# Optimization experiments

Measured on AMD Instinct MI355X. Metric: run time of the kernel, lower is better.

## Reference

```python
import jax, jax.numpy as jnp
import numpy as np

# graph structure constants
G = 64            # num graphs
NPG = 1600        # nodes per graph
N = G * NPG       # 102400 total nodes
EPG = 51200       # edges per graph (avg degree 32)
E = G * EPG       # 3276800 total edges
F_IN = 512
H_OUT = 512
RATIO = 0.8
K = int(np.ceil(RATIO * NPG))   # 1280 kept nodes per graph
NK = G * K


def gcn_conv(x, src, dst, W, b, n, ew):
    """PyG GCNConv: D^-1/2 (A+I) D^-1/2 X W + b, with edge weights ew."""
    h = x @ W
    deg = jax.ops.segment_sum(ew, dst, num_segments=n) + 1.0  # +1 for self loop
    dis = jax.lax.rsqrt(deg)
    norm = dis[src] * dis[dst] * ew                 # [E]
    agg = jax.ops.segment_sum(h[src] * norm[:, None], dst, num_segments=n)
    return agg + h * (dis * dis)[:, None] + b       # self-loop norm = dis_i^2


def setup_inputs() -> dict:
    key = jax.random.key(0)
    k_x, k_e, k_w1, k_wr, k_wo, k_w2 = jax.random.split(key, 6)
    x = jax.random.normal(k_x, (N, F_IN), dtype=jnp.float32)
    # within-graph random edges
    local = jax.random.randint(k_e, (2, G, EPG), 0, NPG, dtype=jnp.int32)
    offs = (jnp.arange(G, dtype=jnp.int32) * NPG)[None, :, None]
    edge_index = (local + offs).reshape(2, E)
    batch = jnp.repeat(jnp.arange(G, dtype=jnp.int32), NPG)
    W1 = jax.random.normal(k_w1, (F_IN, 16), dtype=jnp.float32) * (1.0 / np.sqrt(F_IN))
    b1 = jnp.zeros((16,), jnp.float32)
    Wrel = jax.random.normal(k_wr, (16, 1), dtype=jnp.float32) * 0.25
    brel = jnp.zeros((1,), jnp.float32)
    Wroot = jax.random.normal(k_wo, (16, 1), dtype=jnp.float32) * 0.25
    W2 = jax.random.normal(k_w2, (16, H_OUT), dtype=jnp.float32) * 0.25
    b2 = jnp.zeros((H_OUT,), jnp.float32)
    return {"x": x, "edge_index": edge_index, "batch": batch,
            "W1": W1, "b1": b1, "Wrel": Wrel, "brel": brel,
            "Wroot": Wroot, "W2": W2, "b2": b2}


def reference(x, edge_index, batch, W1, b1, Wrel, brel, Wroot, W2, b2):
    src, dst = edge_index[0], edge_index[1]
    ones_e = jnp.ones((E,), x.dtype)
    # conv1 + relu
    h1 = jax.nn.relu(gcn_conv(x, src, dst, W1, b1, N, ones_e))   # [N,16]
    # SAGPooling score: GraphConv(16,1) = lin_rel(sum_j x_j) + lin_root(x), then tanh
    agg = jax.ops.segment_sum(h1[src], dst, num_segments=N)
    score = jnp.tanh((agg @ Wrel + brel + h1 @ Wroot)[:, 0])      # [N]
    # per-graph top-k (graphs are equal-sized, contiguous)
    vals, idx = jax.lax.top_k(score.reshape(G, NPG), K)           # [G,K]
    perm = (idx + (jnp.arange(G, dtype=idx.dtype) * NPG)[:, None]).reshape(-1)  # [NK]
    xk = h1[perm] * vals.reshape(-1)[:, None]                     # x[perm] * score[perm]
    # filter_adj: keep edges with both endpoints kept, remap indices
    kept = jnp.zeros((N,), bool).at[perm].set(True)
    inv = jnp.zeros((N,), jnp.int32).at[perm].set(jnp.arange(NK, dtype=jnp.int32))
    em = (kept[src] & kept[dst]).astype(x.dtype)                  # weight-0 == dropped edge
    # conv2 + relu on pooled graph
    h2 = jax.nn.relu(gcn_conv(xk, inv[src], inv[dst], W2, b2, NK, em))  # [NK,H]
    # global mean pool (each graph keeps exactly K nodes)
    out = jax.ops.segment_sum(h2, batch[perm], num_segments=G) / K
    return out
```

## Files before the change

kernel.cpp:

```cpp
#include <hip/hip_runtime.h>
#include <math.h>

#define G_    64
#define NPG_  1600
#define N_    (G_*NPG_)
#define EPG_  51200
#define E_    (G_*EPG_)
#define FIN_  512
#define HOUT_ 512
#define KEEP_ 1280

__global__ __launch_bounds__(1024) void k_build(const int* __restrict__ esrc,
                                                const int* __restrict__ edst,
                                                int* __restrict__ offs,
                                                int* __restrict__ rend,
                                                float* __restrict__ dis,
                                                unsigned short* __restrict__ csr) {
  __shared__ __align__(16) unsigned short csrs[EPG_];
  __shared__ int hist[NPG_];
  __shared__ int wsum[16];
  const int g = blockIdx.x, t = threadIdx.x;
  const int lane = t & 63, wid = t >> 6;
  const int eb = g * EPG_, nb = g * NPG_;

  for (int i = t; i < NPG_; i += 1024) hist[i] = 0;
  __syncthreads();
  for (int e = t; e < EPG_; e += 1024) atomicAdd(&hist[edst[eb + e] - nb], 1);
  __syncthreads();

  int c0 = 0, c1 = 0;
  if (t < 800) { c0 = hist[2 * t]; c1 = hist[2 * t + 1]; }
  const int val = c0 + c1;
  int incl = val;
#pragma unroll
  for (int m = 1; m < 64; m <<= 1) {
    const int u = __shfl_up(incl, m);
    if (lane >= m) incl += u;
  }
  if (lane == 63) wsum[wid] = incl;
  __syncthreads();
  int woff = 0;
  for (int w2 = 0; w2 < wid; ++w2) woff += wsum[w2];
  incl += woff;
  if (t < 800) {
    const int excl = incl - val;
    const int p0 = excl, p1 = p0 + c0;
    offs[nb + 2 * t] = eb + p0;     rend[nb + 2 * t] = eb + p1;
    offs[nb + 2 * t + 1] = eb + p1; rend[nb + 2 * t + 1] = eb + p1 + c1;
    dis[nb + 2 * t] = rsqrtf((float)c0 + 1.0f);
    dis[nb + 2 * t + 1] = rsqrtf((float)c1 + 1.0f);
    hist[2 * t] = p0;
    hist[2 * t + 1] = p1;
  }
  __syncthreads();
  for (int e = t; e < EPG_; e += 1024) {
    const int s = esrc[eb + e];
    const int d = edst[eb + e] - nb;
    const int p = atomicAdd(&hist[d], 1);
    csrs[p] = (unsigned short)(s - nb);
  }
  __syncthreads();
  const uint4* s4 = reinterpret_cast<const uint4*>(csrs);
  uint4* d4 = reinterpret_cast<uint4*>(csr + eb);
  for (int i = t; i < EPG_ / 8; i += 1024) d4[i] = s4[i];
}

typedef _Float16 f16x8 __attribute__((ext_vector_type(8)));
typedef float f32x4 __attribute__((ext_vector_type(4)));
#define WSTR_ 520

__global__ __launch_bounds__(256, 4) void k_xw1(const float* __restrict__ x,
                                                const float* __restrict__ W1,
                                                const float* __restrict__ dis,
                                                float* __restrict__ hd) {
  __shared__ _Float16 wls[2][16][WSTR_];
  const int t = threadIdx.x;

  for (int i = t; i < FIN_ * 16; i += 256) {
    const int k = i >> 4, n = i & 15;
    const float w = W1[i];
    const _Float16 w1 = (_Float16)w;
    const float r = w - (float)w1;
    wls[0][n][k] = w1;
    wls[1][n][k] = (_Float16)r;
  }
  __syncthreads();

  const int lane = t & 63, wid = t >> 6;
  const int g = lane >> 4, m = lane & 15;
  const int tile = blockIdx.x * 4 + wid;
  const int rb = tile * 16;

  const float* xrow = x + (size_t)(rb + m) * FIN_ + g * 8;
  const _Float16* wb1 = &wls[0][m][g * 8];
  const _Float16* wb2 = &wls[1][m][g * 8];

  f32x4 acc = {0.f, 0.f, 0.f, 0.f};
#pragma unroll
  for (int t4 = 0; t4 < 16; ++t4) {
    const float4 p0 = *reinterpret_cast<const float4*>(xrow + t4 * 32);
    const float4 p1 = *reinterpret_cast<const float4*>(xrow + t4 * 32 + 4);
    const float xv[8] = {p0.x, p0.y, p0.z, p0.w, p1.x, p1.y, p1.z, p1.w};
    f16x8 a1, a2;
#pragma unroll
    for (int j = 0; j < 8; ++j) {
      const _Float16 h = (_Float16)xv[j];
      a1[j] = h;
      a2[j] = (_Float16)(xv[j] - (float)h);
    }
    const f16x8 b1 = *reinterpret_cast<const f16x8*>(wb1 + t4 * 32);
    const f16x8 b2 = *reinterpret_cast<const f16x8*>(wb2 + t4 * 32);
    acc = __builtin_amdgcn_mfma_f32_16x16x32_f16(a1, b1, acc, 0, 0, 0);
    acc = __builtin_amdgcn_mfma_f32_16x16x32_f16(a1, b2, acc, 0, 0, 0);
    acc = __builtin_amdgcn_mfma_f32_16x16x32_f16(a2, b1, acc, 0, 0, 0);
  }

  const float4 d4 = reinterpret_cast<const float4*>(dis)[(rb >> 2) + g];
  const float dd[4] = {d4.x, d4.y, d4.z, d4.w};
#pragma unroll
  for (int rg = 0; rg < 4; ++rg)
    hd[(size_t)(rb + g * 4 + rg) * 16 + m] = acc[rg] * dd[rg];
}

__global__ __launch_bounds__(1024) void k_conv1l(
    const unsigned short* __restrict__ csr, const int* __restrict__ offs,
    const int* __restrict__ rend, const float* __restrict__ hd,
    const float* __restrict__ dis, const float* __restrict__ b1,
    const float* __restrict__ Wrel, const float* __restrict__ Wroot,
    float* __restrict__ h1, float* __restrict__ rarr, float* __restrict__ tarr) {
  __shared__ float hds[NPG_ * 16];
  const int g = blockIdx.x >> 2, q = blockIdx.x & 3;
  const int nb = g * NPG_;
  const int t = threadIdx.x;
  {
    const float4* src = reinterpret_cast<const float4*>(hd + (size_t)nb * 16);
    float4* dst = reinterpret_cast<float4*>(hds);
    for (int i = t; i < NPG_ * 4; i += 1024) dst[i] = src[i];
  }
  __syncthreads();
  const int c = t & 15;
  const float bb = b1[c], wr = Wrel[c], wo = Wroot[c];
  const int vend = q * 400 + 400;
  for (int vl = q * 400 + (t >> 4); vl < vend; vl += 64) {
    const int v = nb + vl;
    const int rs = offs[v], re = rend[v];
    float acc = 0.f;
    int k = rs;
    for (; k + 4 <= re; k += 4) {
      const int s0 = csr[k], s1 = csr[k + 1];
      const int s2 = csr[k + 2], s3 = csr[k + 3];
      acc += hds[s0 * 16 + c] + hds[s1 * 16 + c];
      acc += hds[s2 * 16 + c] + hds[s3 * 16 + c];
    }
    for (; k < re; ++k) acc += hds[csr[k] * 16 + c];
    const float dd = dis[v];
    float val = fmaf(acc + hds[vl * 16 + c], dd, bb);
    val = fmaxf(val, 0.f);
    h1[(size_t)v * 16 + c] = val;
    float r = val * wr;
    float tt = val * wo;
#pragma unroll
    for (int m = 1; m < 16; m <<= 1) {
      r += __shfl_xor(r, m);
      tt += __shfl_xor(tt, m);
    }
    if (c == 0) { rarr[v] = r; tarr[v] = tt; }
  }
}

__global__ __launch_bounds__(1024) void k_scoretopk(
    const unsigned short* __restrict__ csr, const int* __restrict__ offs,
    const int* __restrict__ rend, const float* __restrict__ rarr,
    const float* __restrict__ tarr, const float* __restrict__ brel,
    const float* __restrict__ h1, int* __restrict__ kept,
    float* __restrict__ dis2, float* __restrict__ h1w,
    float* __restrict__ out) {
  __shared__ float rar[NPG_];
  __shared__ float sar[NPG_];
  __shared__ int   ofs[NPG_];
  __shared__ int   ren[NPG_];
  __shared__ unsigned uu[NPG_];
  __shared__ int   kp[NPG_];
  __shared__ float wv[NPG_];
  __shared__ int   hist[256];
  __shared__ int   part[16];
  __shared__ int   scal[2];

  const int g = blockIdx.x, t = threadIdx.x;
  const int lane = t & 63, wid = t >> 6;
  const int nb = g * NPG_;

  for (int i = t; i < NPG_; i += 1024) {
    rar[i] = rarr[nb + i];
    sar[i] = tarr[nb + i];
    ofs[i] = offs[nb + i];
    ren[i] = rend[nb + i];
  }
  if (t == 0) { scal[0] = 0; scal[1] = KEEP_; }
  __syncthreads();

  const float br = brel[0];
  for (int v = t; v < NPG_; v += 1024) {
    const int rs = ofs[v], re = ren[v];
    float sum = 0.f;
    int k = rs;
    for (; k + 4 <= re; k += 4) {
      sum += rar[csr[k]] + rar[csr[k + 1]];
      sum += rar[csr[k + 2]] + rar[csr[k + 3]];
    }
    for (; k < re; ++k) sum += rar[csr[k]];
    const float s = tanhf(sum + br + sar[v]);
    sar[v] = s;
    const unsigned ub = __float_as_uint(s);
    uu[v] = (ub & 0x80000000u) ? ~ub : (ub | 0x80000000u);
  }
  __syncthreads();

  const unsigned maskTab[4] = {0u, 0xFF000000u, 0xFFFF0000u, 0xFFFFFF00u};
  const int shTab[4] = {24, 16, 8, 0};
  for (int pass = 0; pass < 4; ++pass) {
    const unsigned lo = (unsigned)scal[0];
    const int remc = scal[1];
    const unsigned msk = maskTab[pass];
    const int sh = shTab[pass];
    if (t < 256) hist[t] = 0;
    __syncthreads();
    for (int v = t; v < NPG_; v += 1024) {
      const unsigned u = uu[v];
      if (((u ^ lo) & msk) == 0) atomicAdd(&hist[(u >> sh) & 255], 1);
    }
    __syncthreads();
    int hv = 0;
    if (t < 256) hv = hist[t];
    int incl = hv;
#pragma unroll
    for (int m = 1; m < 64; m <<= 1) {
      const int u2 = __shfl_up(incl, m);
      if (lane >= m) incl += u2;
    }
    if (t < 256 && lane == 63) part[wid] = incl;
    __syncthreads();
    if (t < 256) {
      int woff = 0;
      for (int w2 = 0; w2 < wid; ++w2) woff += part[w2];
      const int tot = part[0] + part[1] + part[2] + part[3];
      const int sb = tot - (incl + woff) + hv;
      const int sb1 = sb - hv;
      if (sb >= remc && sb1 < remc) {
        scal[0] = (int)(lo | ((unsigned)t << sh));
        scal[1] = remc - sb1;
      }
    }
    __syncthreads();
  }
  const unsigned T = (unsigned)scal[0];
  const int remT = scal[1];

  const int i0 = 2 * t, i1 = 2 * t + 1;
  int f0 = 0, f1 = 0;
  if (i0 < NPG_) f0 = (uu[i0] == T);
  if (i1 < NPG_) f1 = (uu[i1] == T);
  int incl2 = f0 + f1;
#pragma unroll
  for (int m = 1; m < 64; m <<= 1) {
    const int u2 = __shfl_up(incl2, m);
    if (lane >= m) incl2 += u2;
  }
  if (lane == 63) part[wid] = incl2;
  __syncthreads();
  int woff2 = 0;
  for (int w2 = 0; w2 < wid; ++w2) woff2 += part[w2];
  const int excl = incl2 + woff2 - (f0 + f1);
  if (i0 < NPG_) kp[i0] = (uu[i0] > T) || (f0 && excl < remT);
  if (i1 < NPG_) kp[i1] = (uu[i1] > T) || (f1 && (excl + f0) < remT);
  __syncthreads();
  for (int v = t; v < NPG_; v += 1024) kept[nb + v] = kp[v];

  for (int v = t; v < NPG_; v += 1024) {
    float w = 0.f;
    if (kp[v]) {
      const int rs = ofs[v], re = ren[v];
      int c2 = 0, k = rs;
      for (; k + 4 <= re; k += 4) {
        c2 += kp[csr[k]] + kp[csr[k + 1]];
        c2 += kp[csr[k + 2]] + kp[csr[k + 3]];
      }
      for (; k < re; ++k) c2 += kp[csr[k]];
      const float d2 = rsqrtf((float)c2 + 1.0f);
      dis2[nb + v] = d2;
      w = sar[v] * d2;
    }
    wv[v] = w;
  }
  if (t < HOUT_) out[g * HOUT_ + t] = 0.f;
  __syncthreads();

  for (int i = t; i < NPG_ * 16; i += 1024)
    h1w[(size_t)nb * 16 + i] = h1[(size_t)nb * 16 + i] * wv[i >> 4];
}

__global__ __launch_bounds__(1024) void k_conv2l(
    const unsigned short* __restrict__ csr, const int* __restrict__ offs,
    const int* __restrict__ rend, const float* __restrict__ h1w,
    const int* __restrict__ kept, const float* __restrict__ dis2,
    float* __restrict__ y16) {
  __shared__ float hds[NPG_ * 16];
  const int g = blockIdx.x >> 2, q = blockIdx.x & 3;
  const int nb = g * NPG_;
  const int t = threadIdx.x;
  {
    const float4* src = reinterpret_cast<const float4*>(h1w + (size_t)nb * 16);
    float4* dst = reinterpret_cast<float4*>(hds);
    for (int i = t; i < NPG_ * 4; i += 1024) dst[i] = src[i];
  }
  __syncthreads();
  const int c = t & 15;
  const int vend = q * 400 + 400;
  for (int vl = q * 400 + (t >> 4); vl < vend; vl += 64) {
    const int v = nb + vl;
    if (!kept[v]) continue;
    const int rs = offs[v], re = rend[v];
    float acc = 0.f;
    int k = rs;
    for (; k + 4 <= re; k += 4) {
      const int s0 = csr[k], s1 = csr[k + 1];
      const int s2 = csr[k + 2], s3 = csr[k + 3];
      acc += hds[s0 * 16 + c] + hds[s1 * 16 + c];
      acc += hds[s2 * 16 + c] + hds[s3 * 16 + c];
    }
    for (; k < re; ++k) acc += hds[csr[k] * 16 + c];
    acc += hds[vl * 16 + c];
    y16[(size_t)v * 16 + c] = acc * dis2[v];
  }
}

__global__ __launch_bounds__(256, 1) void k_gemm2pool(const float* __restrict__ y16,
                                                      const int* __restrict__ kept,
                                                      const float* __restrict__ W2,
                                                      const float* __restrict__ b2,
                                                      float* __restrict__ out) {
  __shared__ float red[256];
  const int blk = blockIdx.x;
  const int g = blk >> 5;
  const int sub = blk & 31;
  const int jbase = (sub & 1) * 256;
  const int nstart = g * NPG_ + (sub >> 1) * 100;
  const int tid = threadIdx.x;
  const int wave = tid >> 6, lane = tid & 63;

  float w[16][4];
#pragma unroll
  for (int k = 0; k < 16; ++k)
#pragma unroll
    for (int c = 0; c < 4; ++c)
      w[k][c] = W2[k * HOUT_ + jbase + lane + c * 64];
  float b2r[4];
#pragma unroll
  for (int c = 0; c < 4; ++c) b2r[c] = b2[jbase + lane + c * 64];

  float acc[4] = {0.f, 0.f, 0.f, 0.f};
  for (int i = wave; i < 100; i += 4) {
    const int v = nstart + i;
    if (!kept[v]) continue;
    const float4* yp = reinterpret_cast<const float4*>(y16 + (size_t)v * 16);
    float4 q0 = yp[0], q1 = yp[1], q2 = yp[2], q3 = yp[3];
    const float yv[16] = {q0.x, q0.y, q0.z, q0.w, q1.x, q1.y, q1.z, q1.w,
                          q2.x, q2.y, q2.z, q2.w, q3.x, q3.y, q3.z, q3.w};
    float z[4] = {b2r[0], b2r[1], b2r[2], b2r[3]};
#pragma unroll
    for (int k = 0; k < 16; ++k)
#pragma unroll
      for (int c = 0; c < 4; ++c)
        z[c] = fmaf(yv[k], w[k][c], z[c]);
#pragma unroll
    for (int c = 0; c < 4; ++c) acc[c] += fmaxf(z[c], 0.f);
  }

  red[tid] = 0.f;
  __syncthreads();
#pragma unroll
  for (int c = 0; c < 4; ++c) atomicAdd(&red[lane + 64 * c], acc[c]);
  __syncthreads();
  atomicAdd(&out[g * HOUT_ + jbase + tid], red[tid] * (1.0f / (float)KEEP_));
}

extern "C" void kernel_launch(void* const* d_in, const int* in_sizes, int n_in,
                              void* d_out, int out_size, void* d_ws, size_t ws_size,
                              hipStream_t stream) {
  (void)in_sizes; (void)n_in; (void)out_size; (void)ws_size;
  const float* x     = (const float*)d_in[0];
  const int*   ei    = (const int*)  d_in[1];
  const float* W1    = (const float*)d_in[3];
  const float* b1    = (const float*)d_in[4];
  const float* Wrel  = (const float*)d_in[5];
  const float* brel  = (const float*)d_in[6];
  const float* Wroot = (const float*)d_in[7];
  const float* W2    = (const float*)d_in[8];
  const float* b2    = (const float*)d_in[9];
  const int* esrc = ei;
  const int* edst = ei + E_;

  char* ws = (char*)d_ws;
  float*          hd    = (float*)(ws);
  float*          h1    = (float*)(ws + 6553600);
  float*          h1w   = (float*)(ws + 13107200);
  float*          y16   = (float*)(ws + 19660800);
  unsigned short* csr   = (unsigned short*)(ws + 26214400);
  int*            offs  = (int*)(ws + 32768000);
  int*            rendp = (int*)(ws + 33177600);
  float*          dis   = (float*)(ws + 33587200);
  int*            kept  = (int*)(ws + 33996800);
  float*          rarr  = (float*)(ws + 34406400);
  float*          tarr  = (float*)(ws + 34816000);
  float*          dis2  = (float*)(ws + 35225600);
  float*          out   = (float*)d_out;

  hipLaunchKernelGGL(k_build,     dim3(G_),    dim3(1024), 0, stream,
                     esrc, edst, offs, rendp, dis, csr);
  hipLaunchKernelGGL(k_xw1,       dim3(1600),  dim3(256),  0, stream,
                     x, W1, dis, hd);
  hipLaunchKernelGGL(k_conv1l,    dim3(256),   dim3(1024), 0, stream,
                     csr, offs, rendp, hd, dis, b1, Wrel, Wroot, h1, rarr, tarr);
  hipLaunchKernelGGL(k_scoretopk, dim3(G_),    dim3(1024), 0, stream,
                     csr, offs, rendp, rarr, tarr, brel, h1, kept, dis2, h1w, out);
  hipLaunchKernelGGL(k_conv2l,    dim3(256),   dim3(1024), 0, stream,
                     csr, offs, rendp, h1w, kept, dis2, y16);
  hipLaunchKernelGGL(k_gemm2pool, dim3(2048),  dim3(256),  0, stream,
                     y16, kept, W2, b2, out);
}
```

Measured before the change: 214.1 us.

## Split score/top-k kernel into score, top-k and post kernels across more blocks

The fused per-graph score/top-k kernel ran only 64 blocks, leaving most CUs idle during the edge-gather phases. It is now split into three kernels: a 320-block score kernel, a 64-block radix top-k kernel that works on precomputed keys, and a 320-block post kernel that computes the pooled-graph degree and scales h1. Scores and keys go through global memory in reused workspace (the hd region), and the change adds two kernel launches.

Result: no change. 214.3 us (+0.1%).

```diff
diff --git a/kernel.cpp b/kernel.cpp
--- a/kernel.cpp
+++ b/kernel.cpp
@@ -168,52 +168,47 @@
   }
 }
 
-__global__ __launch_bounds__(1024) void k_scoretopk(
+__global__ __launch_bounds__(320) void k_score(
     const unsigned short* __restrict__ csr, const int* __restrict__ offs,
     const int* __restrict__ rend, const float* __restrict__ rarr,
     const float* __restrict__ tarr, const float* __restrict__ brel,
-    const float* __restrict__ h1, int* __restrict__ kept,
-    float* __restrict__ dis2, float* __restrict__ h1w,
+    float* __restrict__ scoreg, unsigned* __restrict__ uug) {
+  __shared__ float rar[NPG_];
+  const int g = blockIdx.x / 5, q = blockIdx.x % 5;
+  const int nb = g * NPG_;
+  const int t = threadIdx.x;
+  for (int i = t; i < NPG_; i += 320) rar[i] = rarr[nb + i];
+  __syncthreads();
+  const int vl = q * 320 + t;
+  const int v = nb + vl;
+  const int rs = offs[v], re = rend[v];
+  float sum = 0.f;
+  int k = rs;
+  for (; k + 4 <= re; k += 4) {
+    sum += rar[csr[k]] + rar[csr[k + 1]];
+    sum += rar[csr[k + 2]] + rar[csr[k + 3]];
+  }
+  for (; k < re; ++k) sum += rar[csr[k]];
+  const float s = tanhf(sum + brel[0] + tarr[v]);
+  scoreg[v] = s;
+  const unsigned ub = __float_as_uint(s);
+  uug[v] = (ub & 0x80000000u) ? ~ub : (ub | 0x80000000u);
+}
+
+__global__ __launch_bounds__(1024) void k_topk(
+    const unsigned* __restrict__ uug, int* __restrict__ kept,
     float* __restrict__ out) {
-  __shared__ float rar[NPG_];
-  __shared__ float sar[NPG_];
-  __shared__ int   ofs[NPG_];
-  __shared__ int   ren[NPG_];
   __shared__ unsigned uu[NPG_];
-  __shared__ int   kp[NPG_];
-  __shared__ float wv[NPG_];
-  __shared__ int   hist[256];
-  __shared__ int   part[16];
-  __shared__ int   scal[2];
-
+  __shared__ int kp[NPG_];
+  __shared__ int hist[256];
+  __shared__ int part[16];
+  __shared__ int scal[2];
   const int g = blockIdx.x, t = threadIdx.x;
   const int lane = t & 63, wid = t >> 6;
   const int nb = g * NPG_;
 
-  for (int i = t; i < NPG_; i += 1024) {
-    rar[i] = rarr[nb + i];
-    sar[i] = tarr[nb + i];
-    ofs[i] = offs[nb + i];
-    ren[i] = rend[nb + i];
-  }
+  for (int i = t; i < NPG_; i += 1024) uu[i] = uug[nb + i];
   if (t == 0) { scal[0] = 0; scal[1] = KEEP_; }
-  __syncthreads();
-
-  const float br = brel[0];
-  for (int v = t; v < NPG_; v += 1024) {
-    const int rs = ofs[v], re = ren[v];
-    float sum = 0.f;
-    int k = rs;
-    for (; k + 4 <= re; k += 4) {
-      sum += rar[csr[k]] + rar[csr[k + 1]];
-      sum += rar[csr[k + 2]] + rar[csr[k + 3]];
-    }
-    for (; k < re; ++k) sum += rar[csr[k]];
-    const float s = tanhf(sum + br + sar[v]);
-    sar[v] = s;
-    const unsigned ub = __float_as_uint(s);
-    uu[v] = (ub & 0x80000000u) ? ~ub : (ub | 0x80000000u);
-  }
   __syncthreads();
 
   const unsigned maskTab[4] = {0u, 0xFF000000u, 0xFFFF0000u, 0xFFFFFF00u};
@@ -275,28 +270,41 @@
   if (i1 < NPG_) kp[i1] = (uu[i1] > T) || (f1 && (excl + f0) < remT);
   __syncthreads();
   for (int v = t; v < NPG_; v += 1024) kept[nb + v] = kp[v];
-
-  for (int v = t; v < NPG_; v += 1024) {
-    float w = 0.f;
-    if (kp[v]) {
-      const int rs = ofs[v], re = ren[v];
-      int c2 = 0, k = rs;
-      for (; k + 4 <= re; k += 4) {
-        c2 += kp[csr[k]] + kp[csr[k + 1]];
-        c2 += kp[csr[k + 2]] + kp[csr[k + 3]];
-      }
-      for (; k < re; ++k) c2 += kp[csr[k]];
-      const float d2 = rsqrtf((float)c2 + 1.0f);
-      dis2[nb + v] = d2;
-      w = sar[v] * d2;
-    }
-    wv[v] = w;
-  }
   if (t < HOUT_) out[g * HOUT_ + t] = 0.f;
-  __syncthreads();
-
-  for (int i = t; i < NPG_ * 16; i += 1024)
-    h1w[(size_t)nb * 16 + i] = h1[(size_t)nb * 16 + i] * wv[i >> 4];
+}
+
+__global__ __launch_bounds__(320) void k_post(
+    const unsigned short* __restrict__ csr, const int* __restrict__ offs,
+    const int* __restrict__ rend, const int* __restrict__ kept,
+    const float* __restrict__ scoreg, const float* __restrict__ h1,
+    float* __restrict__ dis2, float* __restrict__ h1w) {
+  __shared__ int kp[NPG_];
+  __shared__ float wvs[320];
+  const int g = blockIdx.x / 5, q = blockIdx.x % 5;
+  const int nb = g * NPG_;
+  const int t = threadIdx.x;
+  for (int i = t; i < NPG_; i += 320) kp[i] = kept[nb + i];
+  __syncthreads();
+  const int vl = q * 320 + t;
+  const int v = nb + vl;
+  float w = 0.f;
+  if (kp[vl]) {
+    const int rs = offs[v], re = rend[v];
+    int c2 = 0, k = rs;
+    for (; k + 4 <= re; k += 4) {
+      c2 += kp[csr[k]] + kp[csr[k + 1]];
+      c2 += kp[csr[k + 2]] + kp[csr[k + 3]];
+    }
+    for (; k < re; ++k) c2 += kp[csr[k]];
+    const float d2 = rsqrtf((float)c2 + 1.0f);
+    dis2[v] = d2;
+    w = scoreg[v] * d2;
+  }
+  wvs[t] = w;
+  __syncthreads();
+  const size_t base = (size_t)(nb + q * 320) * 16;
+  for (int i = t; i < 320 * 16; i += 320)
+    h1w[base + i] = h1[base + i] * wvs[i >> 4];
 }
 
 __global__ __launch_bounds__(1024) void k_conv2l(
@@ -401,19 +409,21 @@
   const int* edst = ei + E_;
 
   char* ws = (char*)d_ws;
-  float*          hd    = (float*)(ws);
-  float*          h1    = (float*)(ws + 6553600);
-  float*          h1w   = (float*)(ws + 13107200);
-  float*          y16   = (float*)(ws + 19660800);
-  unsigned short* csr   = (unsigned short*)(ws + 26214400);
-  int*            offs  = (int*)(ws + 32768000);
-  int*            rendp = (int*)(ws + 33177600);
-  float*          dis   = (float*)(ws + 33587200);
-  int*            kept  = (int*)(ws + 33996800);
-  float*          rarr  = (float*)(ws + 34406400);
-  float*          tarr  = (float*)(ws + 34816000);
-  float*          dis2  = (float*)(ws + 35225600);
-  float*          out   = (float*)d_out;
+  float*          hd     = (float*)(ws);
+  unsigned*       uug    = (unsigned*)(ws);
+  float*          scoreg = (float*)(ws + 409600);
+  float*          h1     = (float*)(ws + 6553600);
+  float*          h1w    = (float*)(ws + 13107200);
+  float*          y16    = (float*)(ws + 19660800);
+  unsigned short* csr    = (unsigned short*)(ws + 26214400);
+  int*            offs   = (int*)(ws + 32768000);
+  int*            rendp  = (int*)(ws + 33177600);
+  float*          dis    = (float*)(ws + 33587200);
+  int*            kept   = (int*)(ws + 33996800);
+  float*          rarr   = (float*)(ws + 34406400);
+  float*          tarr   = (float*)(ws + 34816000);
+  float*          dis2   = (float*)(ws + 35225600);
+  float*          out    = (float*)d_out;
 
   hipLaunchKernelGGL(k_build,     dim3(G_),    dim3(1024), 0, stream,
                      esrc, edst, offs, rendp, dis, csr);
@@ -421,8 +431,12 @@
                      x, W1, dis, hd);
   hipLaunchKernelGGL(k_conv1l,    dim3(256),   dim3(1024), 0, stream,
                      csr, offs, rendp, hd, dis, b1, Wrel, Wroot, h1, rarr, tarr);
-  hipLaunchKernelGGL(k_scoretopk, dim3(G_),    dim3(1024), 0, stream,
-                     csr, offs, rendp, rarr, tarr, brel, h1, kept, dis2, h1w, out);
+  hipLaunchKernelGGL(k_score,     dim3(320),   dim3(320),  0, stream,
+                     csr, offs, rendp, rarr, tarr, brel, scoreg, uug);
+  hipLaunchKernelGGL(k_topk,      dim3(G_),    dim3(1024), 0, stream,
+                     uug, kept, out);
+  hipLaunchKernelGGL(k_post,      dim3(320),   dim3(320),  0, stream,
+                     csr, offs, rendp, kept, scoreg, h1, dis2, h1w);
   hipLaunchKernelGGL(k_conv2l,    dim3(256),   dim3(1024), 0, stream,
                      csr, offs, rendp, h1w, kept, dis2, y16);
   hipLaunchKernelGGL(k_gemm2pool, dim3(2048),  dim3(256),  0, stream,
```
